# Optimization experiments

Hardware: AMD Instinct MI355X
Metric: run time of the kernel (lower is better)

## Reference

```python
import jax, jax.numpy as jnp
import numpy as np

B, L, S, DIM, NH = 4, 1024, 1024, 1024, 16
DH = DIM // NH


def setup_inputs() -> dict:
    key = jax.random.key(0)
    ks = jax.random.split(key, 16)
    std = 0.02
    inp = {
        'q': jax.random.normal(ks[0], (B, L, DIM), jnp.float32),
        'k': jax.random.normal(ks[1], (B, S, DIM), jnp.float32),
        'v': jax.random.normal(ks[2], (B, S, DIM), jnp.float32),
        'attn_mask': jax.random.bernoulli(ks[3], 0.9, (B, L, S)),
        'pos_bias': jax.random.normal(ks[4], (B, NH, L, S), jnp.float32),
        'Wq': jax.random.normal(ks[5], (DIM, DIM), jnp.float32) * std,
        'bq': jnp.zeros((DIM,), jnp.float32),
        'Wk': jax.random.normal(ks[6], (DIM, DIM), jnp.float32) * std,
        'bk': jnp.zeros((DIM,), jnp.float32),
        'Wv': jax.random.normal(ks[7], (DIM, DIM), jnp.float32) * std,
        'bv': jnp.zeros((DIM,), jnp.float32),
        'Wp': jax.random.normal(ks[8], (DIM, DIM), jnp.float32) * std,
        'bp': jnp.zeros((DIM,), jnp.float32),
        'is_causal': 1,
    }
    return inp


def _attention(q, k, v, attn_mask, pos_bias, Wq, bq, Wk, bk, Wv, bv, Wp, bp, is_causal):
    b, l, _ = q.shape
    s = k.shape[1]
    qh = (q @ Wq + bq).reshape(b, l, NH, DH)   # (B,L,nH,dh)
    kh = (k @ Wk + bk).reshape(b, s, NH, DH)
    vh = (v @ Wv + bv).reshape(b, s, NH, DH)

    mask = attn_mask  # (B,L,S) bool
    if is_causal:
        causal = jnp.tril(jnp.ones((l, l), dtype=bool))
        causal = jnp.pad(causal, ((0, 0), (s - l, 0)), constant_values=True)  # (L,S)
        mask = mask & causal[None]
    # rows with no allowed key attend everywhere (matches torch row-fix)
    row_any = mask.any(axis=-1, keepdims=True)
    mask = jnp.where(row_any, mask, True)

    bias = jnp.where(mask[:, None, :, :], pos_bias, -jnp.inf)  # (B,nH,L,S)
    scale = 1.0 / np.sqrt(DH).astype(np.float32)
    scores = jnp.einsum('blhd,bshd->bhls', qh, kh) * scale + bias
    attn = jax.nn.softmax(scores, axis=-1)
    o = jnp.einsum('bhls,bshd->blhd', attn, vh).reshape(b, l, NH * DH)
    return o @ Wp + bp


def reference(q, k, v, attn_mask, pos_bias, Wq, bq, Wk, bk, Wv, bv, Wp, bp, is_causal):
    return _attention(q, k, v, attn_mask, pos_bias, Wq, bq, Wk, bk, Wv, bv, Wp, bp, is_causal)
```

## Files before the change

kernel.cpp:

```cpp
#include <hip/hip_runtime.h>
#include <hip/hip_bf16.h>

typedef __hip_bfloat16 bf16;
typedef __attribute__((ext_vector_type(4))) float  floatx4;
typedef __attribute__((ext_vector_type(8))) short  short8;
typedef __attribute__((ext_vector_type(8))) __bf16 bf16x8;

constexpr int Bc = 4, Lc = 1024, Sc = 1024, DIMc = 1024, NHc = 16, DHc = 64;

template <typename V>
__device__ auto mfma_bf16_sel(V a, V b, floatx4 c, int)
    -> decltype(__builtin_amdgcn_mfma_f32_16x16x32_bf16(a, b, c, 0, 0, 0)) {
  return __builtin_amdgcn_mfma_f32_16x16x32_bf16(a, b, c, 0, 0, 0);
}
template <typename V>
__device__ floatx4 mfma_bf16_sel(V a, V b, floatx4 c, long) {
  bf16x8 a2 = __builtin_bit_cast(bf16x8, a);
  bf16x8 b2 = __builtin_bit_cast(bf16x8, b);
  return __builtin_amdgcn_mfma_f32_16x16x32_bf16(a2, b2, c, 0, 0, 0);
}
__device__ inline floatx4 mfma_bf16(short8 a, short8 b, floatx4 c) {
  return mfma_bf16_sel(a, b, c, 0);
}

__device__ inline void gload16(const bf16* g, bf16* l) {
  __builtin_amdgcn_global_load_lds(
      (const __attribute__((address_space(1))) unsigned int*)g,
      (__attribute__((address_space(3))) unsigned int*)l, 16, 0, 0);
}

union U8 { uint4 u; bf16 h[8]; };

__device__ inline U8 load8cvt(const float* p) {
    float4 f0 = ((const float4*)p)[0];
    float4 f1 = ((const float4*)p)[1];
    U8 t;
    t.h[0] = __float2bfloat16(f0.x); t.h[1] = __float2bfloat16(f0.y);
    t.h[2] = __float2bfloat16(f0.z); t.h[3] = __float2bfloat16(f0.w);
    t.h[4] = __float2bfloat16(f1.x); t.h[5] = __float2bfloat16(f1.y);
    t.h[6] = __float2bfloat16(f1.z); t.h[7] = __float2bfloat16(f1.w);
    return t;
}

__global__ __launch_bounds__(256)
void prep_kernel(const float* __restrict__ q, const float* __restrict__ k,
                 const float* __restrict__ v,
                 const float* __restrict__ Wq, const float* __restrict__ Wk,
                 const float* __restrict__ Wv, const float* __restrict__ Wp,
                 const int* __restrict__ mask, const int* __restrict__ is_causal_p,
                 bf16* __restrict__ qb, bf16* __restrict__ kb,
                 bf16* __restrict__ vb,
                 bf16* __restrict__ wqt, bf16* __restrict__ wkt,
                 bf16* __restrict__ wvt, bf16* __restrict__ wpt,
                 unsigned long long* __restrict__ mbits,
                 int* __restrict__ rowany_g)
{
    __shared__ float tile[64][68];
    const int tid = threadIdx.x;
    int blk = blockIdx.x;

    if (blk < 6144) {
        const float* src = (blk < 2048) ? q : (blk < 4096) ? k : v;
        bf16*        dst = (blk < 2048) ? qb : (blk < 4096) ? kb : vb;
        const int off = (blk & 2047) * 2048 + tid * 8;
        U8 t = load8cvt(src + off);
        *(uint4*)(dst + off) = t.u;
    } else if (blk < 7168) {
        blk -= 6144;
        const int w  = blk >> 8, t2 = blk & 255;
        const float* W  = (w == 0) ? Wq : (w == 1) ? Wk : (w == 2) ? Wv : Wp;
        bf16*        Wt = (w == 0) ? wqt : (w == 1) ? wkt : (w == 2) ? wvt : wpt;
        const int tk = (t2 >> 4) << 6;
        const int tn = (t2 & 15) << 6;
        #pragma unroll
        for (int i = 0; i < 4; ++i) {
            const int r = (tid >> 4) + i * 16;
            const int c = (tid & 15) << 2;
            *(float4*)(&tile[r][c]) =
                *(const float4*)(W + (size_t)(tk + r) * DIMc + tn + c);
        }
        __syncthreads();
        #pragma unroll
        for (int j = 0; j < 2; ++j) {
            const int nn = tid >> 2;
            const int kc = (tid & 3) + j * 4;
            U8 o;
            #pragma unroll
            for (int u = 0; u < 8; ++u)
                o.h[u] = __float2bfloat16(tile[kc * 8 + u][nn]);
            *(uint4*)(Wt + (size_t)(tn + nn) * DIMc + tk + kc * 8) = o.u;
        }
    } else {
        const int mb  = blk - 7168;
        const int rIb = tid >> 4;
        const int w   = tid & 15;
        const int row = mb * 16 + rIb;
        const int l   = row & (Lc - 1);
        const bool causal = (is_causal_p[0] != 0);

        const int4* mr4 = (const int4*)(mask + (size_t)row * Sc + w * 64);
        unsigned long long bits = 0ull;
        #pragma unroll
        for (int i = 0; i < 16; ++i) {
            int4 m4 = mr4[i];
            unsigned long long nib =
                (unsigned long long)((m4.x != 0) | ((m4.y != 0) << 1) |
                                     ((m4.z != 0) << 2) | ((m4.w != 0) << 3));
            bits |= nib << (4 * i);
        }
        mbits[(size_t)row * 16 + w] = bits;

        const int limit = causal ? l : (Sc - 1);
        const int base  = w * 64;
        unsigned long long am;
        if (limit >= base + 63)  am = bits;
        else if (limit < base)   am = 0ull;
        else                     am = bits & ((2ull << (limit - base)) - 1ull);
        unsigned long long red = am;
        #pragma unroll
        for (int d2 = 1; d2 < 16; d2 <<= 1) red |= __shfl_xor(red, d2);
        if (w == 0) rowany_g[row] = (red != 0ull) ? 1 : 0;
    }
}

__global__ __launch_bounds__(256)
void gemm_qkv_kernel(const bf16* __restrict__ qb, const bf16* __restrict__ kb,
                     const bf16* __restrict__ vb,
                     const bf16* __restrict__ wqt, const bf16* __restrict__ wkt,
                     const bf16* __restrict__ wvt,
                     const float* __restrict__ bq, const float* __restrict__ bk,
                     const float* __restrict__ bv,
                     bf16* __restrict__ qh, bf16* __restrict__ kh,
                     bf16* __restrict__ vt)
{
    __shared__ __align__(16) bf16 As[128 * 64];
    __shared__ __align__(16) bf16 Bs[128 * 64];

    const int z = blockIdx.z;
    const bf16*  A    = (z == 0) ? qb  : (z == 1) ? kb  : vb;
    const bf16*  Bt   = (z == 0) ? wqt : (z == 1) ? wkt : wvt;
    const float* bias = (z == 0) ? bq  : (z == 1) ? bk  : bv;
    bf16*        out  = (z == 0) ? qh  : (z == 1) ? kh  : vt;
    const float  scale = (z == 0) ? 0.125f : 1.0f;

    const int tid  = threadIdx.x;
    const int wave = tid >> 6;
    const int lane = tid & 63;
    const int n = lane & 15, g = lane >> 4;
    const int m0 = blockIdx.x * 128;
    const int n0 = blockIdx.y * 128;
    const int wq_m = (wave & 1) * 64, wq_n = (wave >> 1) * 64;

    const int lrow   = lane >> 3;
    const int lchunk = (lane & 7) * 8;

    floatx4 acc[4][4];
    #pragma unroll
    for (int a = 0; a < 4; ++a)
        #pragma unroll
        for (int b2 = 0; b2 < 4; ++b2)
            acc[a][b2] = (floatx4){0.f, 0.f, 0.f, 0.f};

    for (int k0 = 0; k0 < DIMc; k0 += 64) {
        #pragma unroll
        for (int j = 0; j < 4; ++j) {
            const int rbase = j * 32 + wave * 8;
            const int r = rbase + lrow;
            gload16(A  + (size_t)(m0 + r) * DIMc + k0 + lchunk, As + rbase * 64);
            gload16(Bt + (size_t)(n0 + r) * DIMc + k0 + lchunk, Bs + rbase * 64);
        }
        __syncthreads();
        #pragma unroll
        for (int ks = 0; ks < 2; ++ks) {
            short8 af[4], bf_[4];
            #pragma unroll
            for (int t = 0; t < 4; ++t) {
                af[t]  = *(const short8*)(&As[(wq_m + t * 16 + n) * 64 + ks * 32 + g * 8]);
                bf_[t] = *(const short8*)(&Bs[(wq_n + t * 16 + n) * 64 + ks * 32 + g * 8]);
            }
            #pragma unroll
            for (int tm = 0; tm < 4; ++tm)
                #pragma unroll
                for (int tn = 0; tn < 4; ++tn)
                    acc[tm][tn] = mfma_bf16(af[tm], bf_[tn], acc[tm][tn]);
        }
        __syncthreads();
    }

    #pragma unroll
    for (int tn = 0; tn < 4; ++tn) {
        const int col = n0 + wq_n + tn * 16 + n;
        const float bval = bias[col];
        #pragma unroll
        for (int tm = 0; tm < 4; ++tm) {
            #pragma unroll
            for (int r = 0; r < 4; ++r) {
                const int row = m0 + wq_m + tm * 16 + g * 4 + r;
                const float vv = (acc[tm][tn][r] + bval) * scale;
                const int bb = row >> 10, ll = row & (Lc - 1);
                const int hh = col >> 6,  dd = col & 63;
                size_t idx;
                if (z < 2) idx = (((size_t)(bb * NHc + hh) * Lc + ll) * DHc) + dd;
                else       idx = (((size_t)(bb * NHc + hh) * DHc + dd) * Sc) + ll;
                out[idx] = __float2bfloat16(vv);
            }
        }
    }
}

__global__ __launch_bounds__(256)
void gemm_out_kernel(const bf16* __restrict__ A, const bf16* __restrict__ Bt,
                     const float* __restrict__ bias, float* __restrict__ out)
{
    __shared__ __align__(16) bf16 As[128 * 64];
    __shared__ __align__(16) bf16 Bs[128 * 64];

    const int tid  = threadIdx.x;
    const int wave = tid >> 6;
    const int lane = tid & 63;
    const int n = lane & 15, g = lane >> 4;
    const int m0 = blockIdx.x * 128;
    const int n0 = blockIdx.y * 128;
    const int wq_m = (wave & 1) * 64, wq_n = (wave >> 1) * 64;

    const int lrow   = lane >> 3;
    const int lchunk = (lane & 7) * 8;

    floatx4 acc[4][4];
    #pragma unroll
    for (int a = 0; a < 4; ++a)
        #pragma unroll
        for (int b2 = 0; b2 < 4; ++b2)
            acc[a][b2] = (floatx4){0.f, 0.f, 0.f, 0.f};

    for (int k0 = 0; k0 < DIMc; k0 += 64) {
        #pragma unroll
        for (int j = 0; j < 4; ++j) {
            const int rbase = j * 32 + wave * 8;
            const int r = rbase + lrow;
            gload16(A  + (size_t)(m0 + r) * DIMc + k0 + lchunk, As + rbase * 64);
            gload16(Bt + (size_t)(n0 + r) * DIMc + k0 + lchunk, Bs + rbase * 64);
        }
        __syncthreads();
        #pragma unroll
        for (int ks = 0; ks < 2; ++ks) {
            short8 af[4], bf_[4];
            #pragma unroll
            for (int t = 0; t < 4; ++t) {
                af[t]  = *(const short8*)(&As[(wq_m + t * 16 + n) * 64 + ks * 32 + g * 8]);
                bf_[t] = *(const short8*)(&Bs[(wq_n + t * 16 + n) * 64 + ks * 32 + g * 8]);
            }
            #pragma unroll
            for (int tm = 0; tm < 4; ++tm)
                #pragma unroll
                for (int tn = 0; tn < 4; ++tn)
                    acc[tm][tn] = mfma_bf16(af[tm], bf_[tn], acc[tm][tn]);
        }
        __syncthreads();
    }

    #pragma unroll
    for (int tn = 0; tn < 4; ++tn) {
        const int col = n0 + wq_n + tn * 16 + n;
        const float bval = bias[col];
        #pragma unroll
        for (int tm = 0; tm < 4; ++tm) {
            #pragma unroll
            for (int r = 0; r < 4; ++r) {
                const int row = m0 + wq_m + tm * 16 + g * 4 + r;
                out[(size_t)row * DIMc + col] = acc[tm][tn][r] + bval;
            }
        }
    }
}

constexpr int PADk = 72;

__global__ __launch_bounds__(256)
void flash_attn_kernel(const bf16* __restrict__ qh, const bf16* __restrict__ kh,
                       const bf16* __restrict__ vt,
                       const unsigned long long* __restrict__ mbits,
                       const int* __restrict__ rowany_g,
                       const float* __restrict__ pos_bias,
                       const int* __restrict__ is_causal_p, bf16* __restrict__ o)
{
    __shared__ bf16 Ks[64 * PADk];
    __shared__ bf16 Vs[64 * PADk];
    __shared__ bf16 Pw[4][16 * PADk];
    __shared__ int rowany[64];
    __shared__ int hasfix_s;

    const int tid  = threadIdx.x;
    const int lane = tid & 63;
    const int wave = tid >> 6;
    const int n = lane & 15;
    const int g = lane >> 4;

    const int qt = 15 - (blockIdx.x >> 6);
    const int bh = blockIdx.x & 63;
    const int h  = bh & (NHc - 1);
    const int b  = bh >> 4;
    const int l0 = qt * 64;
    const bool causal = (is_causal_p[0] != 0);

    if (tid == 0) hasfix_s = 0;
    __syncthreads();
    if (tid < 64) {
        const int ra = rowany_g[(b << 10) + l0 + tid];
        rowany[tid] = ra;
        if (ra == 0) atomicOr(&hasfix_s, 1);
    }
    __syncthreads();
    const bool hasfix = (hasfix_s != 0);

    const int qrow_frag = l0 + wave * 16 + n;
    const bf16* qp = qh + ((size_t)bh * Lc + qrow_frag) * DHc;
    const short8 qf0 = *(const short8*)(qp + g * 8);
    const short8 qf1 = *(const short8*)(qp + 32 + g * 8);

    const int e0 = tid * 8,        r0a = e0 >> 6, c0a = e0 & 63;
    const int e1 = tid * 8 + 2048, r0b = e1 >> 6, c0b = e1 & 63;
    const bf16* kb0p = kh + ((size_t)bh * Sc + r0a) * DHc + c0a;
    const bf16* kb1p = kh + ((size_t)bh * Sc + r0b) * DHc + c0b;
    const bf16* vb0p = vt + ((size_t)bh * DHc + r0a) * Sc + c0a;
    const bf16* vb1p = vt + ((size_t)bh * DHc + r0b) * Sc + c0b;
    bf16* ksw0 = Ks + r0a * PADk + c0a;
    bf16* ksw1 = Ks + r0b * PADk + c0b;
    bf16* vsw0 = Vs + r0a * PADk + c0a;
    bf16* vsw1 = Vs + r0b * PADk + c0b;

    union F4 { float4 v; float f[4]; };
    const float* brow[4];
    const unsigned long long* mrow[4];
    int limit_r[4]; bool fix_r[4];
    #pragma unroll
    for (int r = 0; r < 4; ++r) {
        const int row = wave * 16 + g * 4 + r;
        const int l = l0 + row;
        brow[r] = pos_bias + ((size_t)bh * Lc + l) * Sc + 4 * n;
        mrow[r] = mbits + ((size_t)(b << 10) + l) * 16;
        limit_r[r] = causal ? l : (Sc - 1);
        fix_r[r] = (rowany[row] == 0);
    }

    floatx4 oacc[4];
    #pragma unroll
    for (int t = 0; t < 4; ++t) oacc[t] = (floatx4){0.f, 0.f, 0.f, 0.f};
    float m_run[4], l_run[4];
    #pragma unroll
    for (int r = 0; r < 4; ++r) { m_run[r] = -3.0e38f; l_run[r] = 0.f; }

    int nchunk = Sc / 64;
    if (causal && !hasfix) nchunk = qt + 1;

    uint4 kr0 = *(const uint4*)(kb0p);
    uint4 kr1 = *(const uint4*)(kb1p);
    uint4 vr0 = *(const uint4*)(vb0p);
    uint4 vr1 = *(const uint4*)(vb1p);
    F4 bcur[4], bnxt[4];
    unsigned long long mcur[4], mnxt[4];
    #pragma unroll
    for (int r = 0; r < 4; ++r) {
        bcur[r].v = *(const float4*)(brow[r]);
        mcur[r]   = mrow[r][0];
    }

    for (int c = 0; c < nchunk; ++c) {
        __syncthreads();
        *(uint4*)ksw0 = kr0;  *(uint4*)ksw1 = kr1;
        *(uint4*)vsw0 = vr0;  *(uint4*)vsw1 = vr1;
        __syncthreads();

        if (c + 1 < nchunk) {
            const size_t ko = (size_t)(c + 1) * 4096;
            const int    vo = (c + 1) * 64;
            kr0 = *(const uint4*)(kb0p + ko);
            kr1 = *(const uint4*)(kb1p + ko);
            vr0 = *(const uint4*)(vb0p + vo);
            vr1 = *(const uint4*)(vb1p + vo);
            #pragma unroll
            for (int r = 0; r < 4; ++r) {
                bnxt[r].v = *(const float4*)(brow[r] + vo);
                mnxt[r]   = mrow[r][c + 1];
            }
        }

        const int s0 = c * 64;

        floatx4 scv[4];
        #pragma unroll
        for (int t = 0; t < 4; ++t)
            scv[t] = (floatx4){bcur[0].f[t], bcur[1].f[t],
                               bcur[2].f[t], bcur[3].f[t]};
        __builtin_amdgcn_s_setprio(1);
        #pragma unroll
        for (int t = 0; t < 4; ++t) {
            const bf16* kp = Ks + (4 * n + t) * PADk + g * 8;
            short8 kb0 = *(const short8*)(kp);
            short8 kb1 = *(const short8*)(kp + 32);
            scv[t] = mfma_bf16(qf0, kb0, scv[t]);
            scv[t] = mfma_bf16(qf1, kb1, scv[t]);
        }
        __builtin_amdgcn_s_setprio(0);

        #pragma unroll
        for (int r = 0; r < 4; ++r) {
            const int row = wave * 16 + g * 4 + r;
            const int nib = (int)((mcur[r] >> (4 * n)) & 15ull);
            float vals[4];
            #pragma unroll
            for (int t = 0; t < 4; ++t) {
                const int s = s0 + 4 * n + t;
                const bool ok = fix_r[r] || (s <= limit_r[r] && ((nib >> t) & 1));
                vals[t] = ok ? scv[t][r] : -3.0e38f;
            }
            float cm = fmaxf(fmaxf(vals[0], vals[1]), fmaxf(vals[2], vals[3]));
            cm = fmaxf(cm, __shfl_xor(cm, 1));
            cm = fmaxf(cm, __shfl_xor(cm, 2));
            cm = fmaxf(cm, __shfl_xor(cm, 4));
            cm = fmaxf(cm, __shfl_xor(cm, 8));
            const float mnew = fmaxf(m_run[r], cm);
            const float alpha = __expf(m_run[r] - mnew);
            float csum = 0.f;
            union PK { uint2 u; bf16 hb[4]; } pk;
            #pragma unroll
            for (int t = 0; t < 4; ++t) {
                const float p = (vals[t] < -1.0e37f) ? 0.f : __expf(vals[t] - mnew);
                csum += p;
                pk.hb[t] = __float2bfloat16(p);
            }
            *(uint2*)(&Pw[wave][(row & 15) * PADk + 4 * n]) = pk.u;
            csum += __shfl_xor(csum, 1);
            csum += __shfl_xor(csum, 2);
            csum += __shfl_xor(csum, 4);
            csum += __shfl_xor(csum, 8);
            l_run[r] = l_run[r] * alpha + csum;
            m_run[r] = mnew;
            #pragma unroll
            for (int t = 0; t < 4; ++t) oacc[t][r] *= alpha;
        }

        __builtin_amdgcn_s_setprio(1);
        #pragma unroll
        for (int sc2 = 0; sc2 < 2; ++sc2) {
            short8 pa = *(const short8*)(Pw[wave] + n * PADk + sc2 * 32 + g * 8);
            #pragma unroll
            for (int t = 0; t < 4; ++t) {
                short8 vb = *(const short8*)(Vs + (16 * t + n) * PADk + sc2 * 32 + g * 8);
                oacc[t] = mfma_bf16(pa, vb, oacc[t]);
            }
        }
        __builtin_amdgcn_s_setprio(0);

        #pragma unroll
        for (int r = 0; r < 4; ++r) { bcur[r] = bnxt[r]; mcur[r] = mnxt[r]; }
    }

    #pragma unroll
    for (int r = 0; r < 4; ++r) {
        const int l = l0 + wave * 16 + g * 4 + r;
        const float inv = 1.f / l_run[r];
        #pragma unroll
        for (int t = 0; t < 4; ++t) {
            const int d = 16 * t + n;
            o[((size_t)(b * Lc + l)) * DIMc + h * DHc + d] =
                __float2bfloat16(oacc[t][r] * inv);
        }
    }
}

extern "C" void kernel_launch(void* const* d_in, const int* in_sizes, int n_in,
                              void* d_out, int out_size, void* d_ws, size_t ws_size,
                              hipStream_t stream)
{
    (void)in_sizes; (void)n_in; (void)out_size; (void)ws_size;

    const float* q        = (const float*)d_in[0];
    const float* k        = (const float*)d_in[1];
    const float* v        = (const float*)d_in[2];
    const int*   mask     = (const int*)d_in[3];
    const float* pos_bias = (const float*)d_in[4];
    const float* Wq = (const float*)d_in[5];
    const float* bq = (const float*)d_in[6];
    const float* Wk = (const float*)d_in[7];
    const float* bk = (const float*)d_in[8];
    const float* Wv = (const float*)d_in[9];
    const float* bv = (const float*)d_in[10];
    const float* Wp = (const float*)d_in[11];
    const float* bp = (const float*)d_in[12];
    const int*   is_causal = (const int*)d_in[13];

    const size_t per = (size_t)Bc * NHc * Lc * DHc;
    const size_t wsz = (size_t)DIMc * DIMc;
    bf16* qh  = (bf16*)d_ws;
    bf16* kh  = qh + per;
    bf16* vt  = kh + per;
    bf16* oh  = vt + per;
    bf16* qb  = oh + per;
    bf16* kb  = qb + per;
    bf16* vb  = kb + per;
    bf16* wqt = vb + per;
    bf16* wkt = wqt + wsz;
    bf16* wvt = wkt + wsz;
    bf16* wpt = wvt + wsz;
    unsigned long long* mbits = (unsigned long long*)(wpt + wsz);
    int* rowany_g = (int*)(mbits + (size_t)Bc * Lc * 16);
    float* outp = (float*)d_out;

    dim3 bb(256);

    prep_kernel<<<7424, bb, 0, stream>>>(q, k, v, Wq, Wk, Wv, Wp, mask, is_causal,
                                         qb, kb, vb, wqt, wkt, wvt, wpt,
                                         mbits, rowany_g);

    dim3 gq(32, 8, 3);
    gemm_qkv_kernel<<<gq, bb, 0, stream>>>(qb, kb, vb, wqt, wkt, wvt,
                                           bq, bk, bv, qh, kh, vt);

    flash_attn_kernel<<<(Bc * NHc) * (Lc / 64), bb, 0, stream>>>(
        qh, kh, vt, mbits, rowany_g, pos_bias, is_causal, oh);

    dim3 gg(32, 8);
    gemm_out_kernel<<<gg, bb, 0, stream>>>(oh, wpt, bp, outp);
}
```

Before: 551.3 us.

## Double-buffer K/V tiles in LDS and permute K rows to avoid bank conflicts

K and V tiles in shared memory now use two buffers. The next chunk's global loads are written into the alternate buffer after the current chunk's compute, so each iteration needs one barrier instead of two. K rows are stored permuted so the QK^T fragment reads contiguous rows (16*t+n) while keeping the column mapping s=4n+t, with a simpler per-thread load mapping. This doubles LDS use for K/V, which may lower occupancy.

Result: slower. 568.6 us (+3.1%).

```diff
diff --git a/kernel.cpp b/kernel.cpp
--- a/kernel.cpp
+++ b/kernel.cpp
@@ -284,8 +284,8 @@
                        const float* __restrict__ pos_bias,
                        const int* __restrict__ is_causal_p, bf16* __restrict__ o)
 {
-    __shared__ bf16 Ks[64 * PADk];
-    __shared__ bf16 Vs[64 * PADk];
+    __shared__ bf16 Ks[2][64 * PADk];
+    __shared__ bf16 Vs[2][64 * PADk];
     __shared__ bf16 Pw[4][16 * PADk];
     __shared__ int rowany[64];
     __shared__ int hasfix_s;
@@ -318,16 +318,19 @@
     const short8 qf0 = *(const short8*)(qp + g * 8);
     const short8 qf1 = *(const short8*)(qp + 32 + g * 8);
 
-    const int e0 = tid * 8,        r0a = e0 >> 6, c0a = e0 & 63;
-    const int e1 = tid * 8 + 2048, r0b = e1 >> 6, c0b = e1 & 63;
-    const bf16* kb0p = kh + ((size_t)bh * Sc + r0a) * DHc + c0a;
-    const bf16* kb1p = kh + ((size_t)bh * Sc + r0b) * DHc + c0b;
-    const bf16* vb0p = vt + ((size_t)bh * DHc + r0a) * Sc + c0a;
-    const bf16* vb1p = vt + ((size_t)bh * DHc + r0b) * Sc + c0b;
-    bf16* ksw0 = Ks + r0a * PADk + c0a;
-    bf16* ksw1 = Ks + r0b * PADk + c0b;
-    bf16* vsw0 = Vs + r0a * PADk + c0a;
-    bf16* vsw1 = Vs + r0b * PADk + c0b;
+    const int r0a = tid >> 3;
+    const int c0  = (tid & 7) * 8;
+    const int r0b = r0a + 32;
+    const int pa_ = ((r0a >> 2) + ((r0a & 3) << 4));
+    const int pb_ = ((r0b >> 2) + ((r0b & 3) << 4));
+    const bf16* kb0p = kh + ((size_t)bh * Sc + r0a) * DHc + c0;
+    const bf16* kb1p = kh + ((size_t)bh * Sc + r0b) * DHc + c0;
+    const bf16* vb0p = vt + ((size_t)bh * DHc + r0a) * Sc + c0;
+    const bf16* vb1p = vt + ((size_t)bh * DHc + r0b) * Sc + c0;
+    const int kofsA = pa_ * PADk + c0;
+    const int kofsB = pb_ * PADk + c0;
+    const int vofsA = r0a * PADk + c0;
+    const int vofsB = r0b * PADk + c0;
 
     union F4 { float4 v; float f[4]; };
     const float* brow[4];
@@ -353,10 +356,16 @@
     int nchunk = Sc / 64;
     if (causal && !hasfix) nchunk = qt + 1;
 
-    uint4 kr0 = *(const uint4*)(kb0p);
-    uint4 kr1 = *(const uint4*)(kb1p);
-    uint4 vr0 = *(const uint4*)(vb0p);
-    uint4 vr1 = *(const uint4*)(vb1p);
+    {
+        uint4 k0r = *(const uint4*)(kb0p);
+        uint4 k1r = *(const uint4*)(kb1p);
+        uint4 v0r = *(const uint4*)(vb0p);
+        uint4 v1r = *(const uint4*)(vb1p);
+        *(uint4*)(&Ks[0][kofsA]) = k0r;
+        *(uint4*)(&Ks[0][kofsB]) = k1r;
+        *(uint4*)(&Vs[0][vofsA]) = v0r;
+        *(uint4*)(&Vs[0][vofsB]) = v1r;
+    }
     F4 bcur[4], bnxt[4];
     unsigned long long mcur[4], mnxt[4];
     #pragma unroll
@@ -364,15 +373,15 @@
         bcur[r].v = *(const float4*)(brow[r]);
         mcur[r]   = mrow[r][0];
     }
-
+    __syncthreads();
+
+    uint4 kr0, kr1, vr0, vr1;
     for (int c = 0; c < nchunk; ++c) {
-        __syncthreads();
-        *(uint4*)ksw0 = kr0;  *(uint4*)ksw1 = kr1;
-        *(uint4*)vsw0 = vr0;  *(uint4*)vsw1 = vr1;
-        __syncthreads();
-
-        if (c + 1 < nchunk) {
-            const size_t ko = (size_t)(c + 1) * 4096;
+        const int cur = c & 1;
+        const bool more = (c + 1 < nchunk);
+
+        if (more) {
+            const size_t ko = (size_t)(c + 1) * (64 * DHc);
             const int    vo = (c + 1) * 64;
             kr0 = *(const uint4*)(kb0p + ko);
             kr1 = *(const uint4*)(kb1p + ko);
@@ -385,8 +394,6 @@
             }
         }
 
-        const int s0 = c * 64;
-
         floatx4 scv[4];
         #pragma unroll
         for (int t = 0; t < 4; ++t)
@@ -395,14 +402,15 @@
         __builtin_amdgcn_s_setprio(1);
         #pragma unroll
         for (int t = 0; t < 4; ++t) {
-            const bf16* kp = Ks + (4 * n + t) * PADk + g * 8;
-            short8 kb0 = *(const short8*)(kp);
-            short8 kb1 = *(const short8*)(kp + 32);
-            scv[t] = mfma_bf16(qf0, kb0, scv[t]);
-            scv[t] = mfma_bf16(qf1, kb1, scv[t]);
+            const bf16* kp = &Ks[cur][(16 * t + n) * PADk + g * 8];
+            short8 kf0 = *(const short8*)(kp);
+            short8 kf1 = *(const short8*)(kp + 32);
+            scv[t] = mfma_bf16(qf0, kf0, scv[t]);
+            scv[t] = mfma_bf16(qf1, kf1, scv[t]);
         }
         __builtin_amdgcn_s_setprio(0);
 
+        const int s0 = c * 64;
         #pragma unroll
         for (int r = 0; r < 4; ++r) {
             const int row = wave * 16 + g * 4 + r;
@@ -446,14 +454,22 @@
             short8 pa = *(const short8*)(Pw[wave] + n * PADk + sc2 * 32 + g * 8);
             #pragma unroll
             for (int t = 0; t < 4; ++t) {
-                short8 vb = *(const short8*)(Vs + (16 * t + n) * PADk + sc2 * 32 + g * 8);
+                short8 vb = *(const short8*)(&Vs[cur][(16 * t + n) * PADk + sc2 * 32 + g * 8]);
                 oacc[t] = mfma_bf16(pa, vb, oacc[t]);
             }
         }
         __builtin_amdgcn_s_setprio(0);
 
-        #pragma unroll
-        for (int r = 0; r < 4; ++r) { bcur[r] = bnxt[r]; mcur[r] = mnxt[r]; }
+        if (more) {
+            const int nxt = cur ^ 1;
+            *(uint4*)(&Ks[nxt][kofsA]) = kr0;
+            *(uint4*)(&Ks[nxt][kofsB]) = kr1;
+            *(uint4*)(&Vs[nxt][vofsA]) = vr0;
+            *(uint4*)(&Vs[nxt][vofsB]) = vr1;
+            #pragma unroll
+            for (int r = 0; r < 4; ++r) { bcur[r] = bnxt[r]; mcur[r] = mnxt[r]; }
+        }
+        __syncthreads();
     }
 
     #pragma unroll
```
